# Optimization experiments

Measured on AMD Instinct MI355X. Metric: run time of the kernel, lower is better.

## Reference

```python
import jax, jax.numpy as jnp
import numpy as np

KS = 3      # kernel_size
PAD = 1     # padding
GROUPS = 4

def _patches(a, H, W):
    # a: [B, C, H+2*PAD, W+2*PAD] -> [B, C, H, W, KS, KS]
    return jnp.stack([
        jnp.stack([a[:, :, i:i + H, j:j + W] for j in range(KS)], axis=-1)
        for i in range(KS)], axis=-2)

def setup_inputs() -> dict:
    key = jax.random.key(0)
    ks = jax.random.split(key, 7)
    B, Cin, Cout, H, W = 8, 256, 256, 64, 64
    std = np.sqrt(2.0 / Cout)  # kaiming fan_out
    return {
        "x": jax.random.normal(ks[0], (B, Cin, H, W), jnp.float32),
        "y": jax.random.normal(ks[1], (B, Cin, H, W), jnp.float32),
        "wq": jax.random.normal(ks[2], (Cout, Cin), jnp.float32) * std,
        "wk": jax.random.normal(ks[3], (Cout, Cin), jnp.float32) * std,
        "wv": jax.random.normal(ks[4], (Cout, Cin), jnp.float32) * std,
        "rel_h": jax.random.normal(ks[5], (Cout // 2, 1, 1, KS, 1), jnp.float32),
        "rel_w": jax.random.normal(ks[6], (Cout // 2, 1, 1, 1, KS), jnp.float32),
    }

def reference(x, y, wq, wk, wv, rel_h, rel_w):
    B, _, H, W = x.shape
    Cout = wq.shape[0]
    half = Cout // 2
    xp = jnp.pad(x, ((0, 0), (0, 0), (PAD, PAD), (PAD, PAD)))
    q = jnp.einsum('oi,bihw->bohw', wq, y)          # [B,Cout,H,W]
    k = jnp.einsum('oi,bihw->bohw', wk, xp)         # [B,Cout,H+2,W+2]
    v = jnp.einsum('oi,bihw->bohw', wv, xp)
    kp = _patches(k, H, W)                          # [B,Cout,H,W,KS,KS]
    vp = _patches(v, H, W)
    kp = jnp.concatenate([kp[:, :half] + rel_h[None], kp[:, half:] + rel_w[None]], axis=1)
    cg = Cout // GROUPS
    kp = kp.reshape(B, GROUPS, cg, H, W, KS * KS)
    vp = vp.reshape(B, GROUPS, cg, H, W, KS * KS)
    qg = q.reshape(B, GROUPS, cg, H, W, 1)
    attn = jax.nn.softmax(qg * kp, axis=-1)         # per-channel softmax over window
    out = jnp.einsum('bnchwk,bnchwk->bnchw', attn, vp)
    return out.reshape(B, Cout, H, W)
```

## Files before the change

kernel.cpp:

```cpp
#include <hip/hip_runtime.h>
#include <hip/hip_bf16.h>
#include <stdint.h>

typedef __attribute__((ext_vector_type(8))) short short8;
typedef __attribute__((ext_vector_type(4))) float floatx4;
typedef __attribute__((ext_vector_type(4))) unsigned int uintx4;
typedef __attribute__((ext_vector_type(2))) unsigned int uintx2;
typedef __attribute__((ext_vector_type(4))) unsigned short ushort4v;
typedef unsigned int u32;

#define HH 64
#define WW 64
#define HWSZ 4096
#define BB 8
#define CIN 256
#define COUT 256
#define NTOT 32768

#define GLL16(g, l)                                                            \
    __builtin_amdgcn_global_load_lds(                                          \
        (const __attribute__((address_space(1))) u32*)(const void*)(g),        \
        (__attribute__((address_space(3))) u32*)(void*)(l), 16, 0, 0)

__device__ __forceinline__ unsigned short f2b(float f) {
    union { float f; unsigned int u; } v; v.f = f;
    unsigned int r = v.u + 0x7FFFu + ((v.u >> 16) & 1u);
    return (unsigned short)(r >> 16);
}
__device__ __forceinline__ float b2f(unsigned short h) {
    union { unsigned int u; float f; } v; v.u = ((unsigned int)h) << 16;
    return v.f;
}

__global__ __launch_bounds__(256) void transpose_cast(
        const float* __restrict__ y, const float* __restrict__ x,
        unsigned short* __restrict__ yT, unsigned short* __restrict__ xT) {
    __shared__ float lt[64 * 65];
    int zz = blockIdx.z;
    int which = zz & 1;
    int b = zz >> 1;
    const float* src = which ? x : y;
    unsigned short* dst = which ? xT : yT;
    int p0 = blockIdx.x * 64;
    int c0 = blockIdx.y * 64;
    int t = threadIdx.x;

    const float* sp = src + ((size_t)b * CIN + c0) * HWSZ + p0;
    int chL = t >> 4;
    int pxL = (t & 15) * 4;
    #pragma unroll
    for (int pass = 0; pass < 4; ++pass) {
        int ch = chL + pass * 16;
        float4 v = *(const float4*)(sp + (size_t)ch * HWSZ + pxL);
        lt[ch * 65 + pxL + 0] = v.x;
        lt[ch * 65 + pxL + 1] = v.y;
        lt[ch * 65 + pxL + 2] = v.z;
        lt[ch * 65 + pxL + 3] = v.w;
    }
    __syncthreads();

    int c8 = (t & 7) * 8;
    int pxR = t >> 3;
    unsigned short* dp = dst + ((size_t)b * HWSZ + p0) * CIN + c0 + c8;
    #pragma unroll
    for (int pass = 0; pass < 2; ++pass) {
        int px = pxR + pass * 32;
        unsigned int dw[4];
        #pragma unroll
        for (int j = 0; j < 4; ++j) {
            float lo = lt[(c8 + 2 * j) * 65 + px];
            float hi = lt[(c8 + 2 * j + 1) * 65 + px];
            dw[j] = (unsigned int)f2b(lo) | ((unsigned int)f2b(hi) << 16);
        }
        *(uintx4*)(dp + (size_t)px * CIN) = (uintx4){dw[0], dw[1], dw[2], dw[3]};
    }
}

__global__ void wcast(const float* __restrict__ wq, const float* __restrict__ wk,
                      const float* __restrict__ wv,
                      unsigned short* __restrict__ wqb, unsigned short* __restrict__ wkb,
                      unsigned short* __restrict__ wvb) {
    int idx = blockIdx.x * 256 + threadIdx.x;
    wqb[idx] = f2b(wq[idx]);
    wkb[idx] = f2b(wk[idx]);
    wvb[idx] = f2b(wv[idx]);
}

__global__ __launch_bounds__(256)
void gemm_qkv(const unsigned short* __restrict__ wqb, const unsigned short* __restrict__ wkb,
              const unsigned short* __restrict__ wvb,
              const unsigned short* __restrict__ yT, const unsigned short* __restrict__ xT,
              unsigned short* __restrict__ Qb, unsigned short* __restrict__ Kb,
              unsigned short* __restrict__ Vb) {
    __shared__ unsigned short lA[128 * 32];
    __shared__ unsigned short lB[128 * 32];

    int z = blockIdx.z;
    const unsigned short* Wb = (z == 0) ? wqb : (z == 1) ? wkb : wvb;
    const unsigned short* In = (z == 0) ? yT : xT;
    unsigned short* Out = (z == 0) ? Qb : (z == 1) ? Kb : Vb;

    int n0 = blockIdx.x * 128;
    int m0 = blockIdx.y * 128;
    int t = threadIdx.x;
    int lane = t & 63;
    int wave = t >> 6;
    int quad = lane >> 4;
    int l16 = lane & 15;
    int wm = (wave >> 1) * 64;
    int wn = (wave & 1) * 64;

    int sA0 = t >> 2;
    int cch = (t & 3) * 8;
    int sB0 = t >> 2;
    int sB1 = 64 + (t >> 2);
    int gnB0 = 4 * (sB0 & 31) + (sB0 >> 5);
    int gnB1 = 4 * (sB1 & 31) + (sB1 >> 5);

    const unsigned short* gA0 = Wb + (size_t)(m0 + sA0) * CIN + cch;
    const unsigned short* gA1 = Wb + (size_t)(m0 + sA0 + 64) * CIN + cch;
    const unsigned short* gB0 = In + (size_t)(n0 + gnB0) * CIN + cch;
    const unsigned short* gB1 = In + (size_t)(n0 + gnB1) * CIN + cch;

    unsigned short* lA0 = lA + wave * 512;
    unsigned short* lA1 = lA + wave * 512 + 2048;
    unsigned short* lB0 = lB + wave * 512;
    unsigned short* lB1 = lB + wave * 512 + 2048;

    floatx4 acc[4][4];
    #pragma unroll
    for (int mi = 0; mi < 4; ++mi)
        #pragma unroll
        for (int ni = 0; ni < 4; ++ni)
            acc[mi][ni] = (floatx4){0.f, 0.f, 0.f, 0.f};

    const unsigned short* rdA[4];
    const unsigned short* rdB[4];
    #pragma unroll
    for (int mi = 0; mi < 4; ++mi)
        rdA[mi] = lA + (wm + mi * 16 + l16) * 32 + quad * 8;
    #pragma unroll
    for (int ni = 0; ni < 4; ++ni)
        rdB[ni] = lB + (ni * 32 + (wn >> 2) + l16) * 32 + quad * 8;

    #pragma unroll
    for (int ks = 0; ks < 8; ++ks) {
        int koff = ks * 32;
        GLL16(gA0 + koff, lA0);
        GLL16(gA1 + koff, lA1);
        GLL16(gB0 + koff, lB0);
        GLL16(gB1 + koff, lB1);
        __syncthreads();

        short8 af[4], bf[4];
        #pragma unroll
        for (int mi = 0; mi < 4; ++mi)
            af[mi] = *(const short8*)rdA[mi];
        #pragma unroll
        for (int ni = 0; ni < 4; ++ni)
            bf[ni] = *(const short8*)rdB[ni];
        #pragma unroll
        for (int mi = 0; mi < 4; ++mi)
            #pragma unroll
            for (int ni = 0; ni < 4; ++ni)
                acc[mi][ni] = __builtin_amdgcn_mfma_f32_16x16x32_bf16(af[mi], bf[ni], acc[mi][ni], 0, 0, 0);
        __syncthreads();
    }

    int colb = n0 + wn + 4 * l16;
    #pragma unroll
    for (int mi = 0; mi < 4; ++mi) {
        #pragma unroll
        for (int r = 0; r < 4; ++r) {
            int row = m0 + wm + mi * 16 + quad * 4 + r;
            unsigned int lo = (unsigned int)f2b(acc[mi][0][r]) | ((unsigned int)f2b(acc[mi][1][r]) << 16);
            unsigned int hi = (unsigned int)f2b(acc[mi][2][r]) | ((unsigned int)f2b(acc[mi][3][r]) << 16);
            *(uintx2*)(Out + (size_t)row * NTOT + colb) = (uintx2){lo, hi};
        }
    }
}

__global__ __launch_bounds__(256)
void attn(const unsigned short* __restrict__ Q,
          const unsigned short* __restrict__ K,
          const unsigned short* __restrict__ V,
          const float* __restrict__ rel_h,
          const float* __restrict__ rel_w,
          float* __restrict__ out) {
    int gid = blockIdx.x * 256 + threadIdx.x;
    int w8 = gid & 7;
    int w0 = w8 << 3;
    int h = (gid >> 3) & 63;
    int c = (gid >> 9) & 255;
    int b = gid >> 17;

    size_t nb = (size_t)c * NTOT + (size_t)b * HWSZ;
    const unsigned short* Kp = K + nb;
    const unsigned short* Vp = V + nb;

    short8 qr = *(const short8*)(Q + nb + h * 64 + w0);
    float q[8];
    #pragma unroll
    for (int i = 0; i < 8; ++i) q[i] = b2f((unsigned short)qr[i]);

    bool use_h = (c < 128);
    float rel3[3];
    if (use_h) {
        rel3[0] = rel_h[c * 3 + 0]; rel3[1] = rel_h[c * 3 + 1]; rel3[2] = rel_h[c * 3 + 2];
    } else {
        int cc = c - 128;
        rel3[0] = rel_w[cc * 3 + 0]; rel3[1] = rel_w[cc * 3 + 1]; rel3[2] = rel_w[cc * 3 + 2];
    }
    float rr[9];
    #pragma unroll
    for (int r = 0; r < 3; ++r)
        #pragma unroll
        for (int j = 0; j < 3; ++j)
            rr[r * 3 + j] = use_h ? rel3[r] : rel3[j];

    float kb[3][10], vb[3][10];
    #pragma unroll
    for (int r = 0; r < 3; ++r) {
        int ih = h + r - 1;
        bool rok = (unsigned)ih < 64u;
        #pragma unroll
        for (int xx = 0; xx < 10; ++xx) { kb[r][xx] = 0.f; vb[r][xx] = 0.f; }
        if (rok) {
            int ro = ih * 64;
            short8 km = *(const short8*)(Kp + ro + w0);
            short8 vm = *(const short8*)(Vp + ro + w0);
            #pragma unroll
            for (int i = 0; i < 8; ++i) {
                kb[r][i + 1] = b2f((unsigned short)km[i]);
                vb[r][i + 1] = b2f((unsigned short)vm[i]);
            }
            if (w0 > 0)  { kb[r][0] = b2f(Kp[ro + w0 - 1]); vb[r][0] = b2f(Vp[ro + w0 - 1]); }
            if (w0 < 56) { kb[r][9] = b2f(Kp[ro + w0 + 8]); vb[r][9] = b2f(Vp[ro + w0 + 8]); }
        }
    }

    float ov[8];
    #pragma unroll
    for (int wi = 0; wi < 8; ++wi) {
        float qv = q[wi];
        float lg[9];
        #pragma unroll
        for (int r = 0; r < 3; ++r)
            #pragma unroll
            for (int j = 0; j < 3; ++j)
                lg[r * 3 + j] = qv * (kb[r][wi + j] + rr[r * 3 + j]);
        float m = lg[0];
        #pragma unroll
        for (int t2 = 1; t2 < 9; ++t2) m = fmaxf(m, lg[t2]);
        float s = 0.f, o = 0.f;
        #pragma unroll
        for (int r = 0; r < 3; ++r)
            #pragma unroll
            for (int j = 0; j < 3; ++j) {
                float e = __expf(lg[r * 3 + j] - m);
                s += e;
                o += e * vb[r][wi + j];
            }
        ov[wi] = o * __builtin_amdgcn_rcpf(s);
    }

    size_t oi = ((size_t)b * COUT + c) * HWSZ + h * 64 + w0;
    *(floatx4*)(out + oi)     = (floatx4){ ov[0], ov[1], ov[2], ov[3] };
    *(floatx4*)(out + oi + 4) = (floatx4){ ov[4], ov[5], ov[6], ov[7] };
}

extern "C" void kernel_launch(void* const* d_in, const int* in_sizes, int n_in,
                              void* d_out, int out_size, void* d_ws, size_t ws_size,
                              hipStream_t stream) {
    const float* x = (const float*)d_in[0];
    const float* y = (const float*)d_in[1];
    const float* wq = (const float*)d_in[2];
    const float* wk = (const float*)d_in[3];
    const float* wv = (const float*)d_in[4];
    const float* rel_h = (const float*)d_in[5];
    const float* rel_w = (const float*)d_in[6];
    float* out = (float*)d_out;

    char* ws = (char*)d_ws;
    unsigned short* yT  = (unsigned short*)(ws);
    unsigned short* xT  = (unsigned short*)(ws + 16777216);
    unsigned short* wqb = (unsigned short*)(ws + 33554432);
    unsigned short* wkb = (unsigned short*)(ws + 33554432 + 131072);
    unsigned short* wvb = (unsigned short*)(ws + 33554432 + 262144);
    unsigned short* Qb  = (unsigned short*)(ws + 33947648);
    unsigned short* Kb  = (unsigned short*)(ws + 33947648 + 16777216);
    unsigned short* Vb  = (unsigned short*)(ws + 33947648 + 33554432);

    transpose_cast<<<dim3(64, 4, 16), 256, 0, stream>>>(y, x, yT, xT);
    wcast<<<256, 256, 0, stream>>>(wq, wk, wv, wqb, wkb, wvb);
    gemm_qkv<<<dim3(256, 2, 3), 256, 0, stream>>>(wqb, wkb, wvb, yT, xT, Qb, Kb, Vb);
    attn<<<4096, 256, 0, stream>>>(Qb, Kb, Vb, rel_h, rel_w, out);
}
```

Measured before the change: 169.3 us.

## Load two K-slices per barrier in QKV GEMM and make attn loads branch-free

The QKV GEMM now stages two 32-wide K slices into separate LDS buffers per iteration, which halves the number of barrier pairs and issues more global-to-LDS loads before each wait. The attention kernel clamps row and edge indices so every K/V load runs unconditionally and then zeroes out-of-range values with selects. This removes divergent branches and lets loads be issued together. The cost is double the LDS footprint and some redundant loads at image borders.

```diff
diff --git a/kernel.cpp b/kernel.cpp
--- a/kernel.cpp
+++ b/kernel.cpp
@@ -6,7 +6,6 @@
 typedef __attribute__((ext_vector_type(4))) float floatx4;
 typedef __attribute__((ext_vector_type(4))) unsigned int uintx4;
 typedef __attribute__((ext_vector_type(2))) unsigned int uintx2;
-typedef __attribute__((ext_vector_type(4))) unsigned short ushort4v;
 typedef unsigned int u32;
 
 #define HH 64
@@ -92,8 +91,8 @@
               const unsigned short* __restrict__ yT, const unsigned short* __restrict__ xT,
               unsigned short* __restrict__ Qb, unsigned short* __restrict__ Kb,
               unsigned short* __restrict__ Vb) {
-    __shared__ unsigned short lA[128 * 32];
-    __shared__ unsigned short lB[128 * 32];
+    __shared__ unsigned short lA[2][128 * 32];
+    __shared__ unsigned short lB[2][128 * 32];
 
     int z = blockIdx.z;
     const unsigned short* Wb = (z == 0) ? wqb : (z == 1) ? wkb : wvb;
@@ -122,11 +121,6 @@
     const unsigned short* gB0 = In + (size_t)(n0 + gnB0) * CIN + cch;
     const unsigned short* gB1 = In + (size_t)(n0 + gnB1) * CIN + cch;
 
-    unsigned short* lA0 = lA + wave * 512;
-    unsigned short* lA1 = lA + wave * 512 + 2048;
-    unsigned short* lB0 = lB + wave * 512;
-    unsigned short* lB1 = lB + wave * 512 + 2048;
-
     floatx4 acc[4][4];
     #pragma unroll
     for (int mi = 0; mi < 4; ++mi)
@@ -134,36 +128,36 @@
         for (int ni = 0; ni < 4; ++ni)
             acc[mi][ni] = (floatx4){0.f, 0.f, 0.f, 0.f};
 
-    const unsigned short* rdA[4];
-    const unsigned short* rdB[4];
-    #pragma unroll
-    for (int mi = 0; mi < 4; ++mi)
-        rdA[mi] = lA + (wm + mi * 16 + l16) * 32 + quad * 8;
-    #pragma unroll
-    for (int ni = 0; ni < 4; ++ni)
-        rdB[ni] = lB + (ni * 32 + (wn >> 2) + l16) * 32 + quad * 8;
-
-    #pragma unroll
-    for (int ks = 0; ks < 8; ++ks) {
-        int koff = ks * 32;
-        GLL16(gA0 + koff, lA0);
-        GLL16(gA1 + koff, lA1);
-        GLL16(gB0 + koff, lB0);
-        GLL16(gB1 + koff, lB1);
+    #pragma unroll
+    for (int it = 0; it < 4; ++it) {
+        int k0 = it * 64;
+        #pragma unroll
+        for (int bsel = 0; bsel < 2; ++bsel) {
+            int ko = k0 + bsel * 32;
+            unsigned short* dA = lA[bsel] + wave * 512;
+            unsigned short* dB = lB[bsel] + wave * 512;
+            GLL16(gA0 + ko, dA);
+            GLL16(gA1 + ko, dA + 2048);
+            GLL16(gB0 + ko, dB);
+            GLL16(gB1 + ko, dB + 2048);
+        }
         __syncthreads();
 
-        short8 af[4], bf[4];
-        #pragma unroll
-        for (int mi = 0; mi < 4; ++mi)
-            af[mi] = *(const short8*)rdA[mi];
-        #pragma unroll
-        for (int ni = 0; ni < 4; ++ni)
-            bf[ni] = *(const short8*)rdB[ni];
-        #pragma unroll
-        for (int mi = 0; mi < 4; ++mi)
+        #pragma unroll
+        for (int bsel = 0; bsel < 2; ++bsel) {
+            short8 af[4], bf[4];
+            #pragma unroll
+            for (int mi = 0; mi < 4; ++mi)
+                af[mi] = *(const short8*)(lA[bsel] + (wm + mi * 16 + l16) * 32 + quad * 8);
             #pragma unroll
             for (int ni = 0; ni < 4; ++ni)
-                acc[mi][ni] = __builtin_amdgcn_mfma_f32_16x16x32_bf16(af[mi], bf[ni], acc[mi][ni], 0, 0, 0);
+                bf[ni] = *(const short8*)(lB[bsel] + (ni * 32 + (wn >> 2) + l16) * 32 + quad * 8);
+            #pragma unroll
+            for (int mi = 0; mi < 4; ++mi)
+                #pragma unroll
+                for (int ni = 0; ni < 4; ++ni)
+                    acc[mi][ni] = __builtin_amdgcn_mfma_f32_16x16x32_bf16(af[mi], bf[ni], acc[mi][ni], 0, 0, 0);
+        }
         __syncthreads();
     }
 
@@ -199,9 +193,6 @@
     const unsigned short* Vp = V + nb;
 
     short8 qr = *(const short8*)(Q + nb + h * 64 + w0);
-    float q[8];
-    #pragma unroll
-    for (int i = 0; i < 8; ++i) q[i] = b2f((unsigned short)qr[i]);
 
     bool use_h = (c < 128);
     float rel3[3];
@@ -218,26 +209,36 @@
         for (int j = 0; j < 3; ++j)
             rr[r * 3 + j] = use_h ? rel3[r] : rel3[j];
 
+    int e0 = (w0 > 0) ? w0 - 1 : 0;
+    int e9 = (w0 < 56) ? w0 + 8 : 63;
+    bool okL = (w0 > 0);
+    bool okR = (w0 < 56);
+
     float kb[3][10], vb[3][10];
     #pragma unroll
     for (int r = 0; r < 3; ++r) {
-        int ih = h + r - 1;
-        bool rok = (unsigned)ih < 64u;
-        #pragma unroll
-        for (int xx = 0; xx < 10; ++xx) { kb[r][xx] = 0.f; vb[r][xx] = 0.f; }
-        if (rok) {
-            int ro = ih * 64;
-            short8 km = *(const short8*)(Kp + ro + w0);
-            short8 vm = *(const short8*)(Vp + ro + w0);
-            #pragma unroll
-            for (int i = 0; i < 8; ++i) {
-                kb[r][i + 1] = b2f((unsigned short)km[i]);
-                vb[r][i + 1] = b2f((unsigned short)vm[i]);
-            }
-            if (w0 > 0)  { kb[r][0] = b2f(Kp[ro + w0 - 1]); vb[r][0] = b2f(Vp[ro + w0 - 1]); }
-            if (w0 < 56) { kb[r][9] = b2f(Kp[ro + w0 + 8]); vb[r][9] = b2f(Vp[ro + w0 + 8]); }
-        }
-    }
+        int ihr = h + r - 1;
+        bool rok = (unsigned)ihr < 64u;
+        int ihc = ihr < 0 ? 0 : (ihr > 63 ? 63 : ihr);
+        int ro = ihc * 64;
+        short8 km = *(const short8*)(Kp + ro + w0);
+        short8 vm = *(const short8*)(Vp + ro + w0);
+        float ke0 = b2f(Kp[ro + e0]), ve0 = b2f(Vp[ro + e0]);
+        float ke9 = b2f(Kp[ro + e9]), ve9 = b2f(Vp[ro + e9]);
+        #pragma unroll
+        for (int i = 0; i < 8; ++i) {
+            kb[r][i + 1] = rok ? b2f((unsigned short)km[i]) : 0.f;
+            vb[r][i + 1] = rok ? b2f((unsigned short)vm[i]) : 0.f;
+        }
+        bool ok0 = rok && okL;
+        bool ok9 = rok && okR;
+        kb[r][0] = ok0 ? ke0 : 0.f;  vb[r][0] = ok0 ? ve0 : 0.f;
+        kb[r][9] = ok9 ? ke9 : 0.f;  vb[r][9] = ok9 ? ve9 : 0.f;
+    }
+
+    float q[8];
+    #pragma unroll
+    for (int i = 0; i < 8; ++i) q[i] = b2f((unsigned short)qr[i]);
 
     float ov[8];
     #pragma unroll
```

Measured after the change: 159.6 us. 5.7% less time.
